# Optimization experiments

Measured on AMD Instinct MI355X. Metric: run time of the kernel, lower is better.

Reference implementation:

```python
import jax, jax.numpy as jnp
import numpy as np

B, C, H, W = 2, 512, 64, 64
S = 2            # scale_factor
HEADS = 8
GROUPS = 32      # assumed GroupNorm groups for group_norm(in_channels)
DK = C // HEADS
SCALE = 1.0 / DK ** 2   # faithful to source: 1/d_k**2
RES = H // S
R = RES * 2 - 1


def setup_inputs() -> dict:
    key = jax.random.key(0)
    ks = jax.random.split(key, 8)
    f = lambda k, shp, s=0.02: jax.random.normal(k, shp, jnp.float32) * s
    return {
        "x": jax.random.normal(ks[0], (B, C, H, W), jnp.float32),
        "q_w": f(ks[1], (C, C, 1, 1)),
        "q_b": jnp.zeros((C,), jnp.float32),
        "kv_w": f(ks[2], (2 * C, C, 1, 1)),
        "kv_b": jnp.zeros((2 * C,), jnp.float32),
        "off1_w": f(ks[3], (C, C, S, S)),
        "off1_b": jnp.zeros((C,), jnp.float32),
        "gn_w": jnp.ones((C,), jnp.float32),
        "gn_b": jnp.zeros((C,), jnp.float32),
        "off2_w": f(ks[4], (2, C, 1, 1)),
        "rpe_table": f(ks[5], (HEADS, R, R), 0.01),
        "proj_w": f(ks[6], (C, C, 1, 1)),
        "proj_b": jnp.zeros((C,), jnp.float32),
    }


def _conv(x, w, b=None, stride=1):
    y = jax.lax.conv_general_dilated(x, w, (stride, stride), 'VALID',
                                     dimension_numbers=('NCHW', 'OIHW', 'NCHW'))
    return y if b is None else y + b[None, :, None, None]


def _group_norm(x, w, b, eps=1e-5):
    n, c, h, wd = x.shape
    xg = x.reshape(n, GROUPS, -1)
    mu = xg.mean(-1, keepdims=True)
    var = xg.var(-1, keepdims=True)
    xg = (xg - mu) * jax.lax.rsqrt(var + eps)
    return xg.reshape(n, c, h, wd) * w[None, :, None, None] + b[None, :, None, None]


def _grid_sample(img, grid):
    # bilinear, align_corners=True; img [B,C,H,W], grid [B,...,2] in (x,y) order
    Bn, Cn, Hn, Wn = img.shape
    gshape = grid.shape[1:-1]
    g = grid.reshape(Bn, -1, 2)
    x = (g[..., 0] + 1.0) * 0.5 * (Wn - 1)
    y = (g[..., 1] + 1.0) * 0.5 * (Hn - 1)
    x0 = jnp.floor(x); y0 = jnp.floor(y)
    wx = (x - x0)[:, None, :]; wy = (y - y0)[:, None, :]
    x0i = jnp.clip(x0.astype(jnp.int32), 0, Wn - 1)
    x1i = jnp.clip(x0i + 1, 0, Wn - 1)
    y0i = jnp.clip(y0.astype(jnp.int32), 0, Hn - 1)
    y1i = jnp.clip(y0i + 1, 0, Hn - 1)
    imf = img.reshape(Bn, Cn, Hn * Wn)
    gat = lambda yi, xi: jnp.take_along_axis(imf, (yi * Wn + xi)[:, None, :], axis=2)
    out = (gat(y0i, x0i) * (1 - wx) * (1 - wy) + gat(y0i, x1i) * wx * (1 - wy)
           + gat(y1i, x0i) * (1 - wx) * wy + gat(y1i, x1i) * wx * wy)
    return out.reshape(Bn, Cn, *gshape)


def _forward(x, q_w, q_b, kv_w, kv_b, off1_w, off1_b, gn_w, gn_b, off2_w,
             rpe_table, proj_w, proj_b):
    l = H * W
    q = _conv(x, q_w, q_b)                                   # [B,C,H,W]
    t = _conv(q, off1_w, off1_b, stride=S)                   # [B,C,h,w]
    t = jax.nn.gelu(_group_norm(t, gn_w, gn_b), approximate=False)
    offset = _conv(t, off2_w).transpose(0, 2, 3, 1)          # [B,h,w,2] (y,x)
    h, w = offset.shape[1], offset.shape[2]
    n = h * w
    # reference points (linspace 0.5..h-0.5, normalized by h-1)
    ry = (jnp.linspace(0.5, h - 0.5, h) / (h - 1.0)) * 2.0 - 1.0
    rx = (jnp.linspace(0.5, w - 0.5, w) / (w - 1.0)) * 2.0 - 1.0
    ref = jnp.stack(jnp.meshgrid(ry, rx, indexing='ij'), -1)  # [h,w,2]
    pos = jnp.clip(offset + ref[None], -1.0, 1.0)             # [B,h,w,2]
    sampled = _grid_sample(x, pos[..., ::-1])                 # [B,C,h,w] (context=x)
    kv = _conv(sampled.reshape(B, C, 1, n), kv_w, kv_b)       # [B,2C,1,n]
    k, v = kv[:, :C], kv[:, C:]
    qf = q.reshape(B * HEADS, DK, l)
    kf = k.reshape(B * HEADS, DK, n)
    vf = v.reshape(B * HEADS, DK, n)
    attn = jnp.einsum('bcm,bcn->bmn', qf, kf) * SCALE         # [B*H, l, n]
    # query grid (arange, normalized by dim-1)
    gy = jnp.arange(H, dtype=jnp.float32) / (H - 1.0) * 2.0 - 1.0
    gx = jnp.arange(W, dtype=jnp.float32) / (W - 1.0) * 2.0 - 1.0
    qg = jnp.stack(jnp.meshgrid(gy, gx, indexing='ij'), -1).reshape(l, 2)
    disp = (qg[None, :, None, :] - pos.reshape(B, 1, n, 2)) * 0.5  # [B,l,n,2]
    rpe = jnp.broadcast_to(rpe_table[None], (B, HEADS, R, R))
    bias = _grid_sample(rpe, disp[..., ::-1])                  # [B,HEADS,l,n]
    attn = jax.nn.softmax(attn + bias.reshape(B * HEADS, l, n), axis=-1)
    out = jnp.einsum('bmn,bcn->bcm', attn, vf).reshape(B, C, H, W)
    return _conv(out, proj_w, proj_b)


def reference(x, q_w, q_b, kv_w, kv_b, off1_w, off1_b, gn_w, gn_b, off2_w,
              rpe_table, proj_w, proj_b):
    return _forward(x, q_w, q_b, kv_w, kv_b, off1_w, off1_b, gn_w, gn_b,
                    off2_w, rpe_table, proj_w, proj_b)
```

## Files before the change

### kernel.cpp

```cpp
#include <hip/hip_runtime.h>
#include <hip/hip_bf16.h>
#include <math.h>

typedef float floatx4 __attribute__((ext_vector_type(4)));
typedef short shortx8 __attribute__((ext_vector_type(8)));
typedef unsigned short ush;

#define NB    2
#define NC    512
#define NL    4096
#define NN    1024
#define NH    8
#define NDK   64
#define NR    63
#define LOG2E 1.44269504f
#define QT_SCALE (1.44269504f/4096.0f)

#define OFF_Q      0u
#define OFF_AO     0u
#define OFF_SMP    2097152u
#define OFF_QT     4194304u
#define OFF_T      6291456u
#define OFF_GS     7340032u
#define OFF_POS    7340160u
#define OFF_KT     7344256u
#define OFF_VV     7868544u
#define OFF_PART   8392832u
#define OFF_TAB4   8392832u

__device__ __forceinline__ ush f2bf(float f) {
    unsigned u = __float_as_uint(f);
    u += 0x7fffu + ((u >> 16) & 1u);
    return (ush)(u >> 16);
}
__device__ __forceinline__ float bf2f(ush h) {
    return __uint_as_float(((unsigned)h) << 16);
}

template<int NP, int BSRC, int OUTMODE>
__global__ __launch_bounds__(256) void gemm_mfma_k(
    const float* __restrict__ A, const void* __restrict__ Bv,
    const float* __restrict__ bias, void* __restrict__ Yv, void* __restrict__ Y2,
    int M, int K, int P, int KS)
{
    __shared__ ush a_hi[128 * 72];
    __shared__ ush b_hi[64 * 72];
    __shared__ ush a_lo[NP == 3 ? 128 * 72 : 64];
    __shared__ ush b_lo[NP == 3 ? 64 * 72 : 64];

    int tid = threadIdx.x;
    int wv = tid >> 6, lane = tid & 63, quad = lane >> 4, l15 = lane & 15;
    int bz = blockIdx.z;
    int b = bz / KS, ks = bz - b * KS;
    int m0 = blockIdx.y * 128, p0 = blockIdx.x * 64;
    int Ksl = K / KS, kbeg = ks * Ksl;

    floatx4 acc[2][4];
    #pragma unroll
    for (int mt = 0; mt < 2; ++mt)
        #pragma unroll
        for (int pt = 0; pt < 4; ++pt) acc[mt][pt] = (floatx4)0.f;

    for (int kc = 0; kc < Ksl; kc += 64) {
        int kg0 = kbeg + kc;
        #pragma unroll
        for (int r = 0; r < 8; ++r) {
            int idx = r * 256 + tid;
            int m = idx >> 4, k4 = (idx & 15) << 2;
            float4 av = *(const float4*)(A + (size_t)(m0 + m) * K + kg0 + k4);
            int o = m * 72 + k4;
            ush h0 = f2bf(av.x), h1 = f2bf(av.y), h2 = f2bf(av.z), h3 = f2bf(av.w);
            a_hi[o] = h0; a_hi[o + 1] = h1; a_hi[o + 2] = h2; a_hi[o + 3] = h3;
            if (NP == 3) {
                a_lo[o]     = f2bf(av.x - bf2f(h0));
                a_lo[o + 1] = f2bf(av.y - bf2f(h1));
                a_lo[o + 2] = f2bf(av.z - bf2f(h2));
                a_lo[o + 3] = f2bf(av.w - bf2f(h3));
            }
        }
        #pragma unroll
        for (int r = 0; r < 8; ++r) {
            int idx = r * 256 + tid;
            int k = idx >> 5, p2 = (idx & 31) << 1;
            float v0, v1;
            if (BSRC == 0) {
                const float* Bp = (const float*)Bv + (size_t)b * K * P;
                float2 t2 = *(const float2*)(Bp + (size_t)(kg0 + k) * P + p0 + p2);
                v0 = t2.x; v1 = t2.y;
            } else if (BSRC == 1) {
                const float* Bp = (const float*)Bv + (size_t)b * NC * NL;
                int kk = kg0 + k;
                int c = kk >> 2, kh = (kk >> 1) & 1, kw = kk & 1;
                int p = p0 + p2;
                int oh = p >> 5, ow = p & 31;
                const float* base = Bp + (size_t)c * NL + (2 * oh + kh) * 64 + kw;
                v0 = base[2 * ow];
                v1 = base[2 * ow + 2];
            } else {
                const ush* Bp = (const ush*)Bv + (size_t)b * K * P;
                unsigned u = *(const unsigned*)(Bp + (size_t)(kg0 + k) * P + p0 + p2);
                v0 = bf2f((ush)(u & 0xffffu));
                v1 = bf2f((ush)(u >> 16));
            }
            ush h0 = f2bf(v0), h1 = f2bf(v1);
            b_hi[p2 * 72 + k] = h0;
            b_hi[(p2 + 1) * 72 + k] = h1;
            if (NP == 3) {
                b_lo[p2 * 72 + k]       = f2bf(v0 - bf2f(h0));
                b_lo[(p2 + 1) * 72 + k] = f2bf(v1 - bf2f(h1));
            }
        }
        __syncthreads();

        shortx8 ah[2][2], al[2][2];
        #pragma unroll
        for (int mt = 0; mt < 2; ++mt)
            #pragma unroll
            for (int kk = 0; kk < 2; ++kk) {
                int o = (wv * 32 + mt * 16 + l15) * 72 + kk * 32 + quad * 8;
                ah[mt][kk] = *(const shortx8*)&a_hi[o];
                if (NP == 3) al[mt][kk] = *(const shortx8*)&a_lo[o];
            }
        #pragma unroll
        for (int pt = 0; pt < 4; ++pt) {
            #pragma unroll
            for (int kk = 0; kk < 2; ++kk) {
                int o = (pt * 16 + l15) * 72 + kk * 32 + quad * 8;
                shortx8 bh = *(const shortx8*)&b_hi[o];
                acc[0][pt] = __builtin_amdgcn_mfma_f32_16x16x32_bf16(ah[0][kk], bh, acc[0][pt], 0, 0, 0);
                acc[1][pt] = __builtin_amdgcn_mfma_f32_16x16x32_bf16(ah[1][kk], bh, acc[1][pt], 0, 0, 0);
                if (NP == 3) {
                    shortx8 bl = *(const shortx8*)&b_lo[o];
                    acc[0][pt] = __builtin_amdgcn_mfma_f32_16x16x32_bf16(ah[0][kk], bl, acc[0][pt], 0, 0, 0);
                    acc[1][pt] = __builtin_amdgcn_mfma_f32_16x16x32_bf16(ah[1][kk], bl, acc[1][pt], 0, 0, 0);
                    acc[0][pt] = __builtin_amdgcn_mfma_f32_16x16x32_bf16(al[0][kk], bh, acc[0][pt], 0, 0, 0);
                    acc[1][pt] = __builtin_amdgcn_mfma_f32_16x16x32_bf16(al[1][kk], bh, acc[1][pt], 0, 0, 0);
                }
            }
        }
        __syncthreads();
    }

    #pragma unroll
    for (int mt = 0; mt < 2; ++mt) {
        #pragma unroll
        for (int reg = 0; reg < 4; ++reg) {
            int m = m0 + wv * 32 + mt * 16 + quad * 4 + reg;
            float bb = (OUTMODE == 2) ? 0.f : bias[m];
            #pragma unroll
            for (int pt = 0; pt < 4; ++pt) {
                int p = p0 + pt * 16 + l15;
                float val = acc[mt][pt][reg] + bb;
                if (OUTMODE == 0) {
                    ((float*)Yv)[(size_t)b * M * P + (size_t)m * P + p] = val;
                } else if (OUTMODE == 2) {
                    ((float*)Yv)[(size_t)(ks * NB + b) * M * P + (size_t)m * P + p] = val;
                } else if (OUTMODE == 3) {
                    ((float*)Yv)[(size_t)b * M * P + (size_t)m * P + p] = val;
                    int h = m >> 6, d = m & 63;
                    ((ush*)Y2)[(((size_t)(b * 8 + h) * 4096) + p) * 64 + d] = f2bf(val * QT_SCALE);
                } else {
                    if (m < 512) {
                        int h = m >> 6, d = m & 63;
                        ((ush*)Yv)[(((size_t)(b * 8 + h) * 1024) + p) * 64 + d] = f2bf(val);
                    } else {
                        int c = m - 512;
                        ((ush*)Y2)[((size_t)(b * 512) + c) * 1024 + p] = f2bf(val);
                    }
                }
            }
        }
    }
}

__global__ __launch_bounds__(256) void reduce_off1_k(const float* __restrict__ part,
                                                     const float* __restrict__ bias,
                                                     float* __restrict__ t)
{
    int i = blockIdx.x * 256 + threadIdx.x;
    float v = part[i] + part[i + 1048576] + part[i + 2097152] + part[i + 3145728];
    t[i] = v + bias[(i >> 10) & 511];
}

__global__ __launch_bounds__(256) void gn_stats_k(const float* __restrict__ T, float* __restrict__ gs)
{
    int bg = blockIdx.x;
    const float* base = T + (size_t)bg * 16384;
    float s = 0.f, ss = 0.f;
    for (int i = threadIdx.x; i < 16384; i += 256) { float v = base[i]; s += v; ss += v * v; }
    #pragma unroll
    for (int off = 32; off >= 1; off >>= 1) { s += __shfl_xor(s, off); ss += __shfl_xor(ss, off); }
    __shared__ float red[8];
    int wv = threadIdx.x >> 6;
    if ((threadIdx.x & 63) == 0) { red[wv * 2] = s; red[wv * 2 + 1] = ss; }
    __syncthreads();
    if (threadIdx.x == 0) {
        float S = red[0] + red[2] + red[4] + red[6];
        float SS = red[1] + red[3] + red[5] + red[7];
        float mu = S / 16384.f;
        float var = SS / 16384.f - mu * mu;
        gs[bg * 2] = mu;
        gs[bg * 2 + 1] = rsqrtf(var + 1e-5f);
    }
}

__global__ __launch_bounds__(256) void gn_gelu_k(float* __restrict__ T, const float* __restrict__ gs,
                                                 const float* __restrict__ gw, const float* __restrict__ gb)
{
    int idx = blockIdx.x * 256 + threadIdx.x;
    int bg = idx >> 14;
    int c = (idx >> 10) & 511;
    float mu = gs[bg * 2], rs = gs[bg * 2 + 1];
    float v = (T[idx] - mu) * rs * gw[c] + gb[c];
    T[idx] = v * 0.5f * (1.f + erff(v * 0.70710678118654752f));
}

__global__ __launch_bounds__(256) void offset_pos_k(const float* __restrict__ T,
                                                    const float* __restrict__ w2,
                                                    float* __restrict__ pos)
{
    int b = blockIdx.x >> 5;
    int og = threadIdx.x & 31;
    int cg = threadIdx.x >> 5;
    int op = ((blockIdx.x & 31) << 5) + og;
    const float* Tb = T + (size_t)b * NC * NN + (size_t)cg * 64 * NN + op;
    float o0 = 0.f, o1 = 0.f;
    #pragma unroll 4
    for (int c = 0; c < 64; ++c) {
        float tv = Tb[(size_t)c * NN];
        o0 += w2[cg * 64 + c] * tv;
        o1 += w2[512 + cg * 64 + c] * tv;
    }
    __shared__ float rs[2][8][32];
    rs[0][cg][og] = o0;
    rs[1][cg][og] = o1;
    __syncthreads();
    if (threadIdx.x < 64) {
        int coord = threadIdx.x >> 5, og2 = threadIdx.x & 31;
        float s = 0.f;
        #pragma unroll
        for (int k = 0; k < 8; ++k) s += rs[coord][k][og2];
        int opf = ((blockIdx.x & 31) << 5) + og2;
        int oh = opf >> 5, ow = opf & 31;
        float ref = (coord == 0) ? ((0.5f + oh) / 31.f * 2.f - 1.f)
                                 : ((0.5f + ow) / 31.f * 2.f - 1.f);
        pos[((size_t)b * 1024 + opf) * 2 + coord] = fminf(fmaxf(s + ref, -1.f), 1.f);
    }
}

__global__ __launch_bounds__(256) void sample_k(const float* __restrict__ x,
                                                const float* __restrict__ pos,
                                                ush* __restrict__ smp)
{
    int idx = blockIdx.x * 256 + threadIdx.x;
    int j = idx & 1023, c = (idx >> 10) & 511, b = idx >> 19;
    float py = pos[(b * 1024 + j) * 2];
    float px = pos[(b * 1024 + j) * 2 + 1];
    float fx = (px + 1.f) * 0.5f * 63.f;
    float fy = (py + 1.f) * 0.5f * 63.f;
    float flx = floorf(fx), fly = floorf(fy);
    float wx = fx - flx, wy = fy - fly;
    int x0 = min(max((int)flx, 0), 63), y0 = min(max((int)fly, 0), 63);
    int x1 = min(x0 + 1, 63),           y1 = min(y0 + 1, 63);
    const float* xb = x + ((size_t)(b * NC + c)) * NL;
    float v00 = xb[y0 * 64 + x0];
    float v01 = xb[y0 * 64 + x1];
    float v10 = xb[y1 * 64 + x0];
    float v11 = xb[y1 * 64 + x1];
    float v = v00 * (1 - wx) * (1 - wy) + v01 * wx * (1 - wy)
            + v10 * (1 - wx) * wy       + v11 * wx * wy;
    smp[idx] = f2bf(v);
}

__global__ __launch_bounds__(256) void tab4_k(const float* __restrict__ rpe,
                                              uint2* __restrict__ tab4)
{
    int i = blockIdx.x * 256 + threadIdx.x;
    int h = i >> 12, y = (i >> 6) & 63, x = i & 63;
    const float* R = rpe + (size_t)h * 3969;
    float v00 = (y < 63 && x < 63)         ? R[y * 63 + x] * LOG2E : 0.f;
    float v01 = (y < 63 && x + 1 < 63)     ? R[y * 63 + x + 1] * LOG2E : 0.f;
    float v10 = (y + 1 < 63 && x < 63)     ? R[(y + 1) * 63 + x] * LOG2E : 0.f;
    float v11 = (y + 1 < 63 && x + 1 < 63) ? R[(y + 1) * 63 + x + 1] * LOG2E : 0.f;
    uint2 o;
    o.x = (unsigned)f2bf(v00) | ((unsigned)f2bf(v01) << 16);
    o.y = (unsigned)f2bf(v10) | ((unsigned)f2bf(v11) << 16);
    tab4[i] = o;
}

__global__ __launch_bounds__(256) void attn_k(
    const ush* __restrict__ qT, const ush* __restrict__ kT,
    const ush* __restrict__ vv, const float* __restrict__ pos,
    const uint2* __restrict__ tab4, ush* __restrict__ ao)
{
    __shared__ __align__(16) char smem[50176];
    ush*   pa     = (ush*)smem;
    uint2* tab_s  = (uint2*)(smem + 9216);
    float* posj15 = (float*)(smem + 41984);
    float* obuf   = (float*)smem;

    int bh = blockIdx.y;
    int b = bh >> 3, h = bh & 7;
    int m0 = blockIdx.x * 64;
    int tid = threadIdx.x;
    int wv = tid >> 6, lane = tid & 63, quad = lane >> 4, l15 = lane & 15;

    const ush* qbase = qT + ((size_t)bh * 4096 + m0 + wv * 16 + l15) * 64 + quad * 8;
    shortx8 qf0 = *(const shortx8*)(qbase);
    shortx8 qf1 = *(const shortx8*)(qbase + 32);

    const uint2* tg = tab4 + (size_t)h * 4096;
    for (int i = tid; i < 4096; i += 256) tab_s[i] = tg[i];
    const float* pb = pos + (size_t)b * 2048;
    for (int i = tid; i < 2048; i += 256) posj15[i] = pb[i] * 15.5f;

    float qy15[4], qx15[4];
    #pragma unroll
    for (int reg = 0; reg < 4; ++reg) {
        int mg = m0 + wv * 16 + quad * 4 + reg;
        qy15[reg] = (float)(mg >> 6) * (31.f / 63.f) + 15.5f;
        qx15[reg] = (float)(mg & 63) * (31.f / 63.f) + 15.5f;
    }

    floatx4 o_acc[4], o_sum;
    #pragma unroll
    for (int dt = 0; dt < 4; ++dt) o_acc[dt] = (floatx4)0.f;
    o_sum = (floatx4)0.f;
    shortx8 vone = {16256, 16256, 16256, 16256, 16256, 16256, 16256, 16256};

    __syncthreads();

    const ush* kbase = kT + (size_t)bh * 1024 * 64;
    const ush* vbase = vv + (size_t)(b * 512 + h * 64) * 1024;

    for (int jc = 0; jc < 16; ++jc) {
        int j0 = jc * 64;
        floatx4 sacc[4];
        #pragma unroll
        for (int jt = 0; jt < 4; ++jt) sacc[jt] = (floatx4)0.f;
        #pragma unroll
        for (int jt = 0; jt < 4; ++jt) {
            const ush* kp = kbase + (size_t)(j0 + jt * 16 + l15) * 64 + quad * 8;
            shortx8 kf0 = *(const shortx8*)kp;
            shortx8 kf1 = *(const shortx8*)(kp + 32);
            sacc[jt] = __builtin_amdgcn_mfma_f32_16x16x32_bf16(qf0, kf0, sacc[jt], 0, 0, 0);
            sacc[jt] = __builtin_amdgcn_mfma_f32_16x16x32_bf16(qf1, kf1, sacc[jt], 0, 0, 0);
        }
        #pragma unroll
        for (int jt = 0; jt < 4; ++jt) {
            int j = j0 + jt * 16 + l15;
            float2 pp = *(const float2*)&posj15[j * 2];
            #pragma unroll
            for (int reg = 0; reg < 4; ++reg) {
                float gy = qy15[reg] - pp.x;
                float gx = qx15[reg] - pp.y;
                float fy = floorf(gy), fx = floorf(gx);
                float wy = gy - fy, wx = gx - fx;
                int y0 = min(max((int)fy, 0), 62);
                int x0 = min(max((int)fx, 0), 62);
                uint2 tw = tab_s[(y0 << 6) + x0];
                float r00 = __uint_as_float(tw.x << 16);
                float r01 = __uint_as_float(tw.x & 0xffff0000u);
                float r10 = __uint_as_float(tw.y << 16);
                float r11 = __uint_as_float(tw.y & 0xffff0000u);
                float bx0 = r00 + wx * (r01 - r00);
                float bx1 = r10 + wx * (r11 - r10);
                float p = exp2f(sacc[jt][reg] + (bx0 + wy * (bx1 - bx0)));
                pa[(wv * 16 + quad * 4 + reg) * 72 + jt * 16 + l15] = f2bf(p);
            }
        }
        const ush* pbase = pa + (wv * 16 + l15) * 72 + quad * 8;
        shortx8 pf0 = *(const shortx8*)pbase;
        shortx8 pf1 = *(const shortx8*)(pbase + 32);
        o_sum = __builtin_amdgcn_mfma_f32_16x16x32_bf16(pf0, vone, o_sum, 0, 0, 0);
        o_sum = __builtin_amdgcn_mfma_f32_16x16x32_bf16(pf1, vone, o_sum, 0, 0, 0);
        #pragma unroll
        for (int dt = 0; dt < 4; ++dt) {
            const ush* vp = vbase + (size_t)(dt * 16 + l15) * 1024 + j0 + quad * 8;
            shortx8 vf0 = *(const shortx8*)vp;
            shortx8 vf1 = *(const shortx8*)(vp + 32);
            o_acc[dt] = __builtin_amdgcn_mfma_f32_16x16x32_bf16(pf0, vf0, o_acc[dt], 0, 0, 0);
            o_acc[dt] = __builtin_amdgcn_mfma_f32_16x16x32_bf16(pf1, vf1, o_acc[dt], 0, 0, 0);
        }
    }

    __syncthreads();
    float inv[4];
    #pragma unroll
    for (int reg = 0; reg < 4; ++reg) inv[reg] = 1.f / o_sum[reg];
    #pragma unroll
    for (int dt = 0; dt < 4; ++dt)
        #pragma unroll
        for (int reg = 0; reg < 4; ++reg)
            obuf[(dt * 16 + l15) * 68 + wv * 16 + quad * 4 + reg] = o_acc[dt][reg] * inv[reg];
    __syncthreads();
    ush* aobase = ao + ((size_t)(b * 512 + h * 64)) * 4096 + m0;
    for (int i = tid; i < 4096; i += 256) {
        int d = i >> 6, m = i & 63;
        aobase[(size_t)d * 4096 + m] = f2bf(obuf[d * 68 + m]);
    }
}

extern "C" void kernel_launch(void* const* d_in, const int* in_sizes, int n_in,
                              void* d_out, int out_size, void* d_ws, size_t ws_size,
                              hipStream_t stream) {
    const float* x      = (const float*)d_in[0];
    const float* q_w    = (const float*)d_in[1];
    const float* q_b    = (const float*)d_in[2];
    const float* kv_w   = (const float*)d_in[3];
    const float* kv_b   = (const float*)d_in[4];
    const float* off1_w = (const float*)d_in[5];
    const float* off1_b = (const float*)d_in[6];
    const float* gn_w   = (const float*)d_in[7];
    const float* gn_b   = (const float*)d_in[8];
    const float* off2_w = (const float*)d_in[9];
    const float* rpe    = (const float*)d_in[10];
    const float* proj_w = (const float*)d_in[11];
    const float* proj_b = (const float*)d_in[12];

    float* ws   = (float*)d_ws;
    float* q    = ws + OFF_Q;
    ush*   ao   = (ush*)(ws + OFF_AO);
    ush*   smp  = (ush*)(ws + OFF_SMP);
    ush*   qT   = (ush*)(ws + OFF_QT);
    float* t    = ws + OFF_T;
    float* gs   = ws + OFF_GS;
    float* pos  = ws + OFF_POS;
    ush*   kT   = (ush*)(ws + OFF_KT);
    ush*   vv   = (ush*)(ws + OFF_VV);
    float* part = ws + OFF_PART;
    uint2* tab4 = (uint2*)(ws + OFF_TAB4);
    float* out  = (float*)d_out;

    gemm_mfma_k<3, 0, 3><<<dim3(64, 4, 2), 256, 0, stream>>>(q_w, x, q_b, q, qT, 512, 512, 4096, 1);
    gemm_mfma_k<3, 1, 2><<<dim3(16, 4, 8), 256, 0, stream>>>(off1_w, q, nullptr, part, nullptr, 512, 2048, 1024, 4);
    reduce_off1_k<<<4096, 256, 0, stream>>>(part, off1_b, t);
    gn_stats_k<<<64, 256, 0, stream>>>(t, gs);
    gn_gelu_k<<<4096, 256, 0, stream>>>(t, gs, gn_w, gn_b);
    offset_pos_k<<<64, 256, 0, stream>>>(t, off2_w, pos);
    tab4_k<<<128, 256, 0, stream>>>(rpe, tab4);
    sample_k<<<4096, 256, 0, stream>>>(x, pos, smp);
    gemm_mfma_k<1, 2, 4><<<dim3(16, 8, 2), 256, 0, stream>>>(kv_w, smp, kv_b, kT, vv, 1024, 512, 1024, 1);
    attn_k<<<dim3(64, 16), 256, 0, stream>>>(qT, kT, vv, pos, tab4, ao);
    gemm_mfma_k<1, 2, 0><<<dim3(64, 4, 2), 256, 0, stream>>>(proj_w, ao, proj_b, out, nullptr, 512, 512, 4096, 1);
}
```

Baseline: 365.9 us.

## Software-pipeline QK^T with bias eval and precompute bilinear deltas in RPE table

```diff
diff --git a/kernel.cpp b/kernel.cpp
--- a/kernel.cpp
+++ b/kernel.cpp
@@ -282,13 +282,14 @@
     float v01 = (y < 63 && x + 1 < 63)     ? R[y * 63 + x + 1] * LOG2E : 0.f;
     float v10 = (y + 1 < 63 && x < 63)     ? R[(y + 1) * 63 + x] * LOG2E : 0.f;
     float v11 = (y + 1 < 63 && x + 1 < 63) ? R[(y + 1) * 63 + x + 1] * LOG2E : 0.f;
+    float dx = v01 - v00, dy = v10 - v00, dxy = v11 - v10 - v01 + v00;
     uint2 o;
-    o.x = (unsigned)f2bf(v00) | ((unsigned)f2bf(v01) << 16);
-    o.y = (unsigned)f2bf(v10) | ((unsigned)f2bf(v11) << 16);
-    tab4[i] = o;
-}
-
-__global__ __launch_bounds__(256) void attn_k(
+    o.x = (unsigned)f2bf(v00) | ((unsigned)f2bf(dx) << 16);
+    o.y = (unsigned)f2bf(dy)  | ((unsigned)f2bf(dxy) << 16);
+    tab4[(h << 12) + (y << 6) + (x ^ (y & 15))] = o;
+}
+
+__global__ __launch_bounds__(256, 3) void attn_k(
     const ush* __restrict__ qT, const ush* __restrict__ kT,
     const ush* __restrict__ vv, const float* __restrict__ pos,
     const uint2* __restrict__ tab4, ush* __restrict__ ao)
@@ -304,6 +305,8 @@
     int m0 = blockIdx.x * 64;
     int tid = threadIdx.x;
     int wv = tid >> 6, lane = tid & 63, quad = lane >> 4, l15 = lane & 15;
+    int swz = (quad >> 1) & 1;
+    int effq = quad ^ ((l15 >> 3) << 1);
 
     const ush* qbase = qT + ((size_t)bh * 4096 + m0 + wv * 16 + l15) * 64 + quad * 8;
     shortx8 qf0 = *(const shortx8*)(qbase);
@@ -314,13 +317,11 @@
     const float* pb = pos + (size_t)b * 2048;
     for (int i = tid; i < 2048; i += 256) posj15[i] = pb[i] * 15.5f;
 
-    float qy15[4], qx15[4];
-    #pragma unroll
-    for (int reg = 0; reg < 4; ++reg) {
-        int mg = m0 + wv * 16 + quad * 4 + reg;
-        qy15[reg] = (float)(mg >> 6) * (31.f / 63.f) + 15.5f;
-        qx15[reg] = (float)(mg & 63) * (31.f / 63.f) + 15.5f;
-    }
+    float qy = (float)(m0 >> 6) * (31.f / 63.f) + 15.5f;
+    float qx15[4];
+    #pragma unroll
+    for (int reg = 0; reg < 4; ++reg)
+        qx15[reg] = (float)(wv * 16 + quad * 4 + reg) * (31.f / 63.f) + 15.5f;
 
     floatx4 o_acc[4], o_sum;
     #pragma unroll
@@ -328,60 +329,97 @@
     o_sum = (floatx4)0.f;
     shortx8 vone = {16256, 16256, 16256, 16256, 16256, 16256, 16256, 16256};
 
-    __syncthreads();
-
     const ush* kbase = kT + (size_t)bh * 1024 * 64;
     const ush* vbase = vv + (size_t)(b * 512 + h * 64) * 1024;
-
-    for (int jc = 0; jc < 16; ++jc) {
-        int j0 = jc * 64;
-        floatx4 sacc[4];
-        #pragma unroll
-        for (int jt = 0; jt < 4; ++jt) sacc[jt] = (floatx4)0.f;
+    int wrow = wv * 16 + quad * 4;
+
+    auto loadK0 = [&](shortx8 k0[4], shortx8 k1[4], int j0) {
         #pragma unroll
         for (int jt = 0; jt < 4; ++jt) {
             const ush* kp = kbase + (size_t)(j0 + jt * 16 + l15) * 64 + quad * 8;
-            shortx8 kf0 = *(const shortx8*)kp;
-            shortx8 kf1 = *(const shortx8*)(kp + 32);
-            sacc[jt] = __builtin_amdgcn_mfma_f32_16x16x32_bf16(qf0, kf0, sacc[jt], 0, 0, 0);
-            sacc[jt] = __builtin_amdgcn_mfma_f32_16x16x32_bf16(qf1, kf1, sacc[jt], 0, 0, 0);
-        }
+            k0[jt] = *(const shortx8*)kp;
+            k1[jt] = *(const shortx8*)(kp + 32);
+        }
+    };
+    auto qkT = [&](floatx4 s[4], shortx8 k0[4], shortx8 k1[4]) {
+        #pragma unroll
+        for (int jt = 0; jt < 4; ++jt) s[jt] = (floatx4)0.f;
+        #pragma unroll
+        for (int jt = 0; jt < 4; ++jt) {
+            s[jt] = __builtin_amdgcn_mfma_f32_16x16x32_bf16(qf0, k0[jt], s[jt], 0, 0, 0);
+            s[jt] = __builtin_amdgcn_mfma_f32_16x16x32_bf16(qf1, k1[jt], s[jt], 0, 0, 0);
+        }
+    };
+    auto loadV = [&](shortx8 vf[4][2], int j0) {
+        #pragma unroll
+        for (int dt = 0; dt < 4; ++dt) {
+            const ush* vp = vbase + (size_t)(dt * 16 + l15) * 1024 + j0 + quad * 8;
+            vf[dt][0] = *(const shortx8*)vp;
+            vf[dt][1] = *(const shortx8*)(vp + 32);
+        }
+    };
+    auto evalT = [&](floatx4 s[4], int j0) {
         #pragma unroll
         for (int jt = 0; jt < 4; ++jt) {
             int j = j0 + jt * 16 + l15;
             float2 pp = *(const float2*)&posj15[j * 2];
+            float gy = qy - pp.x;
+            int y0 = (int)gy;
+            float wy = gy - (float)y0;
+            int rbase = (y0 << 6), rs = y0 & 15;
+            int colw = ((jt ^ swz) << 4) + l15;
             #pragma unroll
             for (int reg = 0; reg < 4; ++reg) {
-                float gy = qy15[reg] - pp.x;
                 float gx = qx15[reg] - pp.y;
-                float fy = floorf(gy), fx = floorf(gx);
-                float wy = gy - fy, wx = gx - fx;
-                int y0 = min(max((int)fy, 0), 62);
-                int x0 = min(max((int)fx, 0), 62);
-                uint2 tw = tab_s[(y0 << 6) + x0];
-                float r00 = __uint_as_float(tw.x << 16);
-                float r01 = __uint_as_float(tw.x & 0xffff0000u);
-                float r10 = __uint_as_float(tw.y << 16);
-                float r11 = __uint_as_float(tw.y & 0xffff0000u);
-                float bx0 = r00 + wx * (r01 - r00);
-                float bx1 = r10 + wx * (r11 - r10);
-                float p = exp2f(sacc[jt][reg] + (bx0 + wy * (bx1 - bx0)));
-                pa[(wv * 16 + quad * 4 + reg) * 72 + jt * 16 + l15] = f2bf(p);
-            }
-        }
-        const ush* pbase = pa + (wv * 16 + l15) * 72 + quad * 8;
+                int x0 = (int)gx;
+                float wx = gx - (float)x0;
+                uint2 tw = tab_s[rbase + (x0 ^ rs)];
+                float v00 = __uint_as_float(tw.x << 16);
+                float dx  = __uint_as_float(tw.x & 0xffff0000u);
+                float dy  = __uint_as_float(tw.y << 16);
+                float dxy = __uint_as_float(tw.y & 0xffff0000u);
+                float bx  = fmaf(wx, dx, v00 + s[jt][reg]);
+                float t   = fmaf(wx, dxy, dy);
+                float p = __builtin_amdgcn_exp2f(fmaf(wy, t, bx));
+                pa[(wrow + reg) * 72 + colw] = f2bf(p);
+            }
+        }
+    };
+    auto pvT = [&](shortx8 vf[4][2]) {
+        const ush* pbase = pa + (wv * 16 + l15) * 72 + effq * 8;
         shortx8 pf0 = *(const shortx8*)pbase;
         shortx8 pf1 = *(const shortx8*)(pbase + 32);
         o_sum = __builtin_amdgcn_mfma_f32_16x16x32_bf16(pf0, vone, o_sum, 0, 0, 0);
         o_sum = __builtin_amdgcn_mfma_f32_16x16x32_bf16(pf1, vone, o_sum, 0, 0, 0);
         #pragma unroll
         for (int dt = 0; dt < 4; ++dt) {
-            const ush* vp = vbase + (size_t)(dt * 16 + l15) * 1024 + j0 + quad * 8;
-            shortx8 vf0 = *(const shortx8*)vp;
-            shortx8 vf1 = *(const shortx8*)(vp + 32);
-            o_acc[dt] = __builtin_amdgcn_mfma_f32_16x16x32_bf16(pf0, vf0, o_acc[dt], 0, 0, 0);
-            o_acc[dt] = __builtin_amdgcn_mfma_f32_16x16x32_bf16(pf1, vf1, o_acc[dt], 0, 0, 0);
-        }
+            o_acc[dt] = __builtin_amdgcn_mfma_f32_16x16x32_bf16(pf0, vf[dt][0], o_acc[dt], 0, 0, 0);
+            o_acc[dt] = __builtin_amdgcn_mfma_f32_16x16x32_bf16(pf1, vf[dt][1], o_acc[dt], 0, 0, 0);
+        }
+    };
+
+    shortx8 kA0[4], kA1[4], kB0[4], kB1[4];
+    floatx4 sA[4], sB[4];
+    loadK0(kA0, kA1, 0);
+    __syncthreads();
+    qkT(sA, kA0, kA1);
+    loadK0(kB0, kB1, 64);
+
+    for (int it = 0; it < 8; ++it) {
+        int j0 = it * 128;
+        shortx8 vf[4][2];
+        loadV(vf, j0);
+        qkT(sB, kB0, kB1);
+        if (it < 7) loadK0(kA0, kA1, j0 + 128);
+        evalT(sA, j0);
+        pvT(vf);
+        loadV(vf, j0 + 64);
+        if (it < 7) {
+            qkT(sA, kA0, kA1);
+            loadK0(kB0, kB1, j0 + 192);
+        }
+        evalT(sB, j0 + 64);
+        pvT(vf);
     }
 
     __syncthreads();
```

Result: slower. 432.8 us (+18.3%).

## Software-pipeline K/V loads and QK^T, precompute bilinear deltas, swizzle LDS tables

Applied to the files above, without the earlier changes.

```diff
diff --git a/kernel.cpp b/kernel.cpp
--- a/kernel.cpp
+++ b/kernel.cpp
@@ -282,13 +282,78 @@
     float v01 = (y < 63 && x + 1 < 63)     ? R[y * 63 + x + 1] * LOG2E : 0.f;
     float v10 = (y + 1 < 63 && x < 63)     ? R[(y + 1) * 63 + x] * LOG2E : 0.f;
     float v11 = (y + 1 < 63 && x + 1 < 63) ? R[(y + 1) * 63 + x + 1] * LOG2E : 0.f;
+    float dx = v01 - v00, dy = v10 - v00, dxy = v11 - v10 - v01 + v00;
     uint2 o;
-    o.x = (unsigned)f2bf(v00) | ((unsigned)f2bf(v01) << 16);
-    o.y = (unsigned)f2bf(v10) | ((unsigned)f2bf(v11) << 16);
-    tab4[i] = o;
-}
-
-__global__ __launch_bounds__(256) void attn_k(
+    o.x = (unsigned)f2bf(v00) | ((unsigned)f2bf(dx) << 16);
+    o.y = (unsigned)f2bf(dy)  | ((unsigned)f2bf(dxy) << 16);
+    tab4[(h << 12) + (y << 6) + (x ^ (y & 15))] = o;
+}
+
+#define LOADK_M(K0, K1, J0) do {                                              \
+    _Pragma("unroll")                                                         \
+    for (int jt = 0; jt < 4; ++jt) {                                          \
+        const ush* kp_ = kbase + (size_t)((J0) + jt * 16 + l15) * 64 + quad * 8; \
+        K0[jt] = *(const shortx8*)kp_;                                        \
+        K1[jt] = *(const shortx8*)(kp_ + 32);                                 \
+    } } while (0)
+
+#define QKT_M(S, K0, K1) do {                                                 \
+    _Pragma("unroll")                                                         \
+    for (int jt = 0; jt < 4; ++jt) S[jt] = (floatx4)0.f;                      \
+    _Pragma("unroll")                                                         \
+    for (int jt = 0; jt < 4; ++jt) {                                          \
+        S[jt] = __builtin_amdgcn_mfma_f32_16x16x32_bf16(qf0, K0[jt], S[jt], 0, 0, 0); \
+        S[jt] = __builtin_amdgcn_mfma_f32_16x16x32_bf16(qf1, K1[jt], S[jt], 0, 0, 0); \
+    } } while (0)
+
+#define LOADV_M(VF0, VF1, J0) do {                                            \
+    _Pragma("unroll")                                                         \
+    for (int dt = 0; dt < 4; ++dt) {                                          \
+        const ush* vp_ = vbase + (size_t)(dt * 16 + l15) * 1024 + (J0) + quad * 8; \
+        VF0[dt] = *(const shortx8*)vp_;                                       \
+        VF1[dt] = *(const shortx8*)(vp_ + 32);                                \
+    } } while (0)
+
+#define EVAL_M(S, J0) do {                                                    \
+    _Pragma("unroll")                                                         \
+    for (int jt = 0; jt < 4; ++jt) {                                          \
+        int j_ = (J0) + jt * 16 + l15;                                        \
+        float2 pp_ = *(const float2*)&posj15[j_ * 2];                         \
+        float gy_ = qy - pp_.x;                                               \
+        int y0_ = (int)gy_;                                                   \
+        float wy_ = gy_ - (float)y0_;                                         \
+        int rbase_ = (y0_ << 6), rsw_ = y0_ & 15;                             \
+        int colw_ = ((jt ^ swz) << 4) + l15;                                  \
+        _Pragma("unroll")                                                     \
+        for (int reg = 0; reg < 4; ++reg) {                                   \
+            float gx_ = qx15[reg] - pp_.y;                                    \
+            int x0_ = (int)gx_;                                               \
+            float wx_ = gx_ - (float)x0_;                                     \
+            uint2 tw_ = tab_s[rbase_ + (x0_ ^ rsw_)];                         \
+            float v00_ = __uint_as_float(tw_.x << 16);                        \
+            float dx_  = __uint_as_float(tw_.x & 0xffff0000u);                \
+            float dy_  = __uint_as_float(tw_.y << 16);                        \
+            float dxy_ = __uint_as_float(tw_.y & 0xffff0000u);                \
+            float bx_  = fmaf(wx_, dx_, v00_ + S[jt][reg]);                   \
+            float t_   = fmaf(wx_, dxy_, dy_);                                \
+            float p_ = __builtin_amdgcn_exp2f(fmaf(wy_, t_, bx_));            \
+            pa[(wrow + reg) * 72 + colw_] = f2bf(p_);                         \
+        }                                                                     \
+    } } while (0)
+
+#define PV_M(VF0, VF1) do {                                                   \
+    const ush* pbase_ = pa + (wv * 16 + l15) * 72 + effq * 8;                 \
+    shortx8 pf0_ = *(const shortx8*)pbase_;                                   \
+    shortx8 pf1_ = *(const shortx8*)(pbase_ + 32);                            \
+    o_sum = __builtin_amdgcn_mfma_f32_16x16x32_bf16(pf0_, vone, o_sum, 0, 0, 0); \
+    o_sum = __builtin_amdgcn_mfma_f32_16x16x32_bf16(pf1_, vone, o_sum, 0, 0, 0); \
+    _Pragma("unroll")                                                         \
+    for (int dt = 0; dt < 4; ++dt) {                                          \
+        o_acc[dt] = __builtin_amdgcn_mfma_f32_16x16x32_bf16(pf0_, VF0[dt], o_acc[dt], 0, 0, 0); \
+        o_acc[dt] = __builtin_amdgcn_mfma_f32_16x16x32_bf16(pf1_, VF1[dt], o_acc[dt], 0, 0, 0); \
+    } } while (0)
+
+__global__ __launch_bounds__(256, 3) void attn_k(
     const ush* __restrict__ qT, const ush* __restrict__ kT,
     const ush* __restrict__ vv, const float* __restrict__ pos,
     const uint2* __restrict__ tab4, ush* __restrict__ ao)
@@ -304,6 +369,8 @@
     int m0 = blockIdx.x * 64;
     int tid = threadIdx.x;
     int wv = tid >> 6, lane = tid & 63, quad = lane >> 4, l15 = lane & 15;
+    int swz = (quad >> 1) & 1;
+    int effq = quad ^ ((l15 >> 3) << 1);
 
     const ush* qbase = qT + ((size_t)bh * 4096 + m0 + wv * 16 + l15) * 64 + quad * 8;
     shortx8 qf0 = *(const shortx8*)(qbase);
@@ -314,13 +381,11 @@
     const float* pb = pos + (size_t)b * 2048;
     for (int i = tid; i < 2048; i += 256) posj15[i] = pb[i] * 15.5f;
 
-    float qy15[4], qx15[4];
-    #pragma unroll
-    for (int reg = 0; reg < 4; ++reg) {
-        int mg = m0 + wv * 16 + quad * 4 + reg;
-        qy15[reg] = (float)(mg >> 6) * (31.f / 63.f) + 15.5f;
-        qx15[reg] = (float)(mg & 63) * (31.f / 63.f) + 15.5f;
-    }
+    float qy = (float)(m0 >> 6) * (31.f / 63.f) + 15.5f;
+    float qx15[4];
+    #pragma unroll
+    for (int reg = 0; reg < 4; ++reg)
+        qx15[reg] = (float)(wv * 16 + quad * 4 + reg) * (31.f / 63.f) + 15.5f;
 
     floatx4 o_acc[4], o_sum;
     #pragma unroll
@@ -328,60 +393,32 @@
     o_sum = (floatx4)0.f;
     shortx8 vone = {16256, 16256, 16256, 16256, 16256, 16256, 16256, 16256};
 
-    __syncthreads();
-
     const ush* kbase = kT + (size_t)bh * 1024 * 64;
     const ush* vbase = vv + (size_t)(b * 512 + h * 64) * 1024;
-
-    for (int jc = 0; jc < 16; ++jc) {
-        int j0 = jc * 64;
-        floatx4 sacc[4];
-        #pragma unroll
-        for (int jt = 0; jt < 4; ++jt) sacc[jt] = (floatx4)0.f;
-        #pragma unroll
-        for (int jt = 0; jt < 4; ++jt) {
-            const ush* kp = kbase + (size_t)(j0 + jt * 16 + l15) * 64 + quad * 8;
-            shortx8 kf0 = *(const shortx8*)kp;
-            shortx8 kf1 = *(const shortx8*)(kp + 32);
-            sacc[jt] = __builtin_amdgcn_mfma_f32_16x16x32_bf16(qf0, kf0, sacc[jt], 0, 0, 0);
-            sacc[jt] = __builtin_amdgcn_mfma_f32_16x16x32_bf16(qf1, kf1, sacc[jt], 0, 0, 0);
+    int wrow = wv * 16 + quad * 4;
+
+    shortx8 kA0[4], kA1[4], kB0[4], kB1[4];
+    floatx4 sA[4], sB[4];
+    shortx8 vf0[4], vf1[4];
+    LOADK_M(kA0, kA1, 0);
+    __syncthreads();
+    QKT_M(sA, kA0, kA1);
+    LOADK_M(kB0, kB1, 64);
+
+    for (int it = 0; it < 8; ++it) {
+        int j0 = it * 128;
+        LOADV_M(vf0, vf1, j0);
+        QKT_M(sB, kB0, kB1);
+        if (it < 7) LOADK_M(kA0, kA1, j0 + 128);
+        EVAL_M(sA, j0);
+        PV_M(vf0, vf1);
+        LOADV_M(vf0, vf1, j0 + 64);
+        if (it < 7) {
+            QKT_M(sA, kA0, kA1);
+            LOADK_M(kB0, kB1, j0 + 192);
         }
-        #pragma unroll
-        for (int jt = 0; jt < 4; ++jt) {
-            int j = j0 + jt * 16 + l15;
-            float2 pp = *(const float2*)&posj15[j * 2];
-            #pragma unroll
-            for (int reg = 0; reg < 4; ++reg) {
-                float gy = qy15[reg] - pp.x;
-                float gx = qx15[reg] - pp.y;
-                float fy = floorf(gy), fx = floorf(gx);
-                float wy = gy - fy, wx = gx - fx;
-                int y0 = min(max((int)fy, 0), 62);
-                int x0 = min(max((int)fx, 0), 62);
-                uint2 tw = tab_s[(y0 << 6) + x0];
-                float r00 = __uint_as_float(tw.x << 16);
-                float r01 = __uint_as_float(tw.x & 0xffff0000u);
-                float r10 = __uint_as_float(tw.y << 16);
-                float r11 = __uint_as_float(tw.y & 0xffff0000u);
-                float bx0 = r00 + wx * (r01 - r00);
-                float bx1 = r10 + wx * (r11 - r10);
-                float p = exp2f(sacc[jt][reg] + (bx0 + wy * (bx1 - bx0)));
-                pa[(wv * 16 + quad * 4 + reg) * 72 + jt * 16 + l15] = f2bf(p);
-            }
-        }
-        const ush* pbase = pa + (wv * 16 + l15) * 72 + quad * 8;
-        shortx8 pf0 = *(const shortx8*)pbase;
-        shortx8 pf1 = *(const shortx8*)(pbase + 32);
-        o_sum = __builtin_amdgcn_mfma_f32_16x16x32_bf16(pf0, vone, o_sum, 0, 0, 0);
-        o_sum = __builtin_amdgcn_mfma_f32_16x16x32_bf16(pf1, vone, o_sum, 0, 0, 0);
-        #pragma unroll
-        for (int dt = 0; dt < 4; ++dt) {
-            const ush* vp = vbase + (size_t)(dt * 16 + l15) * 1024 + j0 + quad * 8;
-            shortx8 vf0 = *(const shortx8*)vp;
-            shortx8 vf1 = *(const shortx8*)(vp + 32);
-            o_acc[dt] = __builtin_amdgcn_mfma_f32_16x16x32_bf16(pf0, vf0, o_acc[dt], 0, 0, 0);
-            o_acc[dt] = __builtin_amdgcn_mfma_f32_16x16x32_bf16(pf1, vf1, o_acc[dt], 0, 0, 0);
-        }
+        EVAL_M(sB, j0 + 64);
+        PV_M(vf0, vf1);
     }
 
     __syncthreads();
```

After: 446.8 us. 1.22x slower.
